# Kernel tuning notes

Measured on AMD Instinct MI355X. Metric: run time of the kernel, lower is better.

Reference implementation:

```python
import jax, jax.numpy as jnp
import numpy as np

O = 100000   # num objects
R = 1000000  # num triplets
D = 128      # per-slot feature dim (input_dim[0]=input_dim[1]=input_dim[2])
SUM_D = 3 * D  # MLP in/out width
H = 256      # hidden_dim


def setup_inputs() -> dict:
    key = jax.random.key(0)
    k1, k2, k3, k4, k5 = jax.random.split(key, 5)
    object_feats = jax.random.normal(k1, (O, D), dtype=jnp.float32)
    relation_feats = jax.random.normal(k2, (R, D), dtype=jnp.float32)
    triplet = jax.random.randint(k3, (R, 3), 0, O, dtype=jnp.int64)
    # MLP: Linear(SUM_D->H) + ReLU + Linear(H->SUM_D), kaiming-normal init
    W1 = jax.random.normal(k4, (SUM_D, H), dtype=jnp.float32) * np.sqrt(2.0 / SUM_D)
    b1 = jnp.zeros((H,), dtype=jnp.float32)
    W2 = jax.random.normal(k5, (H, SUM_D), dtype=jnp.float32) * np.sqrt(2.0 / H)
    b2 = jnp.zeros((SUM_D,), dtype=jnp.float32)
    return {
        "object_feats": object_feats,
        "relation_feats": relation_feats,
        "W1": W1, "b1": b1, "W2": W2, "b2": b2,
        "triplet": triplet,
        "triplet_len": R,
    }


def reference(object_feats, relation_feats, W1, b1, W2, b2, triplet, triplet_len):
    t = triplet[:triplet_len]                      # [R, 3]
    subs = t[:, 0]                                 # [R]
    objs = t[:, 1]                                 # [R]
    # gather subj/obj feats, concat with relation feats -> [R, 3D]
    gcn_feat = jnp.concatenate(
        [object_feats[subs], relation_feats, object_feats[objs]], axis=1)
    # 2-layer MLP
    h = jax.nn.relu(gcn_feat @ W1 + b1)            # [R, H]
    out = h @ W2 + b2                              # [R, 3D]
    sub_out = out[:, :D]
    rel_out = out[:, D:-D]
    obj_out = out[:, -D:]
    # scatter-add back to object nodes, then mean by degree, plus residual
    acc = jnp.zeros_like(object_feats)
    acc = acc.at[subs].add(sub_out).at[objs].add(obj_out)   # [O, D]
    one = jnp.ones((triplet_len,), dtype=object_feats.dtype)
    cnt = jnp.zeros((object_feats.shape[0],), dtype=object_feats.dtype)
    cnt = cnt.at[subs].add(one).at[objs].add(one)           # [O]
    output_feat = acc / jnp.clip(cnt, 1.0)[:, None] + object_feats
    return (output_feat, rel_out, triplet, triplet_len)
```

## Files before the change

### kernel.cpp

```cpp
#include <hip/hip_runtime.h>

#define O_N 100000
#define R_N 1000000
#define DIM 128
#define SD 384
#define HD 256
#define BR 64
#define NT (R_N / BR)
#define OBJ8 (O_N * DIM / 8)

typedef __attribute__((ext_vector_type(8))) short short8;
typedef __attribute__((ext_vector_type(4))) float f32x4;

static __device__ __forceinline__ unsigned short f2bf(float x) {
    union { float f; unsigned int u; } v; v.f = x;
    unsigned int r = v.u + 0x7FFFu + ((v.u >> 16) & 1u);
    return (unsigned short)(r >> 16);
}
static __device__ __forceinline__ unsigned long long pack4(f32x4 v) {
    return  (unsigned long long)f2bf(v.x)
         | ((unsigned long long)f2bf(v.y) << 16)
         | ((unsigned long long)f2bf(v.z) << 32)
         | ((unsigned long long)f2bf(v.w) << 48);
}

__global__ void prep_weights(const float* __restrict__ W1, const float* __restrict__ W2,
                             unsigned short* __restrict__ W1T, unsigned short* __restrict__ W2T) {
    int i = blockIdx.x * 256 + threadIdx.x;
    if (i < SD * HD) {
        int h = i / SD, k = i - h * SD;
        W1T[i] = f2bf(W1[k * HD + h]);
    } else {
        int j = i - SD * HD;
        int c = j / HD, k = j - c * HD;
        W2T[j] = f2bf(W2[k * SD + c]);
    }
}

__global__ void conv_obj(const float* __restrict__ objF, unsigned short* __restrict__ objBF) {
    int i = blockIdx.x * 256 + threadIdx.x;
    if (i < OBJ8) {
        f32x4 v0 = ((const f32x4*)(objF + (size_t)i * 8))[0];
        f32x4 v1 = ((const f32x4*)(objF + (size_t)i * 8))[1];
        unsigned long long* dd = (unsigned long long*)(objBF + (size_t)i * 8);
        dd[0] = pack4(v0);
        dd[1] = pack4(v1);
    }
}

__global__ void trip_cnt(const int* __restrict__ trip, float* __restrict__ tripOut,
                         float* __restrict__ lenOut, float* __restrict__ cnt,
                         const int* __restrict__ tlen) {
    int i = blockIdx.x * 256 + threadIdx.x;
    if (i < R_N) {
        int s = trip[3 * i], o = trip[3 * i + 1], t2 = trip[3 * i + 2];
        tripOut[3 * i]     = (float)s;
        tripOut[3 * i + 1] = (float)o;
        tripOut[3 * i + 2] = (float)t2;
        atomicAdd(&cnt[min(max(s, 0), O_N - 1)], 1.0f);
        atomicAdd(&cnt[min(max(o, 0), O_N - 1)], 1.0f);
        if (i == 0) lenOut[0] = (float)tlen[0];
    }
}

__global__ __launch_bounds__(256, 3)
void gemm1_kernel(const unsigned short* __restrict__ objBF, const float* __restrict__ relF,
                  const unsigned short* __restrict__ W1T, const float* __restrict__ b1,
                  const int* __restrict__ trip, unsigned char* __restrict__ hbfB) {
    __shared__ __align__(16) unsigned char Xso[32768];
    __shared__ __align__(16) unsigned char Xsr[16384];
    __shared__ int idxBuf[128];

    const int tid  = threadIdx.x;
    const int lane = tid & 63;
    const int w    = tid >> 6;
    const int r0   = blockIdx.x * BR;
    const int l15  = lane & 15;
    const int l4   = lane >> 4;
    const int hW   = w * 64;

    if (tid < 2 * BR) {
        int rr = r0 + (tid & (BR - 1));
        idxBuf[tid] = min(max(trip[3 * rr + (tid >> 6)], 0), O_N - 1);
    }
    __syncthreads();

    #pragma unroll
    for (int it = 0; it < 8; ++it) {
        int a   = it * 256 + tid;
        int row = a >> 5;
        int q   = a & 31;
        int u   = q ^ (row & 15);
        const unsigned short* src =
            objBF + (size_t)((q < 16) ? idxBuf[row] : idxBuf[BR + row]) * DIM + (u & 15) * 8;
        __builtin_amdgcn_global_load_lds(
            (const __attribute__((address_space(1))) void*)src,
            (__attribute__((address_space(3))) void*)(Xso + it * 4096 + w * 1024),
            16, 0, 0);
    }
    #pragma unroll
    for (int it = 0; it < 4; ++it) {
        int a2  = it * 256 + tid;
        int row = a2 >> 4;
        int j   = a2 & 15;
        const float* rp = relF + (size_t)(r0 + row) * DIM + j * 8;
        f32x4 v0 = ((const f32x4*)rp)[0];
        f32x4 v1 = ((const f32x4*)rp)[1];
        union { unsigned long long q[2]; short8 v; } u;
        u.q[0] = pack4(v0); u.q[1] = pack4(v1);
        *(short8*)(Xsr + row * 256 + ((j ^ (row & 15)) << 4)) = u.v;
    }
    __syncthreads();

    f32x4 acc1[4][4];
    #pragma unroll
    for (int a = 0; a < 4; ++a)
        #pragma unroll
        for (int b = 0; b < 4; ++b) acc1[a][b] = (f32x4)0.0f;

    #pragma unroll
    for (int ks = 0; ks < 12; ++ks) {
        int k0 = ks * 32;
        short8 af[4], bfr[4];
        #pragma unroll
        for (int mh = 0; mh < 4; ++mh)
            af[mh] = *(const short8*)(W1T + (hW + mh * 16 + l15) * SD + k0 + 8 * l4);
        #pragma unroll
        for (int nr = 0; nr < 4; ++nr) {
            int rel = nr * 16 + l15;
            int sw  = rel & 15;
            const unsigned char* p;
            if (ks < 4)       p = Xso + rel * 512 + (((ks * 4 + l4) ^ sw) << 4);
            else if (ks < 8)  p = Xsr + rel * 256 + ((((ks - 4) * 4 + l4) ^ sw) << 4);
            else              p = Xso + rel * 512 + 256 + ((((ks - 8) * 4 + l4) ^ sw) << 4);
            bfr[nr] = *(const short8*)p;
        }
        #pragma unroll
        for (int mh = 0; mh < 4; ++mh)
            #pragma unroll
            for (int nr = 0; nr < 4; ++nr)
                acc1[mh][nr] = __builtin_amdgcn_mfma_f32_16x16x32_bf16(
                    af[mh], bfr[nr], acc1[mh][nr], 0, 0, 0);
    }

    #pragma unroll
    for (int mh = 0; mh < 4; ++mh) {
        int hbase = hW + mh * 16 + 4 * l4;
        float bb0 = b1[hbase], bb1 = b1[hbase + 1], bb2 = b1[hbase + 2], bb3 = b1[hbase + 3];
        int hb   = hbase >> 3;
        int half = (hbase >> 2) & 1;
        #pragma unroll
        for (int nr = 0; nr < 4; ++nr) {
            int rel = nr * 16 + l15;
            unsigned long long pk =
                  (unsigned long long)f2bf(fmaxf(acc1[mh][nr][0] + bb0, 0.f))
                | ((unsigned long long)f2bf(fmaxf(acc1[mh][nr][1] + bb1, 0.f)) << 16)
                | ((unsigned long long)f2bf(fmaxf(acc1[mh][nr][2] + bb2, 0.f)) << 32)
                | ((unsigned long long)f2bf(fmaxf(acc1[mh][nr][3] + bb3, 0.f)) << 48);
            *(unsigned long long*)(hbfB + (size_t)(r0 + rel) * 512
                                   + ((hb ^ (rel & 15)) << 4) + half * 8) = pk;
        }
    }
}

__global__ __launch_bounds__(256, 3)
void gemm2_kernel(const unsigned char* __restrict__ hbfB,
                  const unsigned short* __restrict__ W2T, const float* __restrict__ b2,
                  const int* __restrict__ trip,
                  float* __restrict__ accB, float* __restrict__ relOut) {
    __shared__ __align__(16) unsigned char Hs[32768];
    __shared__ int idxBuf[128];

    const int tid  = threadIdx.x;
    const int lane = tid & 63;
    const int w    = tid >> 6;
    const int r0   = blockIdx.x * BR;
    const int l15  = lane & 15;
    const int l4   = lane >> 4;
    const int cW   = w * 96;

    if (tid < 2 * BR) {
        int rr = r0 + (tid & (BR - 1));
        idxBuf[tid] = min(max(trip[3 * rr + (tid >> 6)], 0), O_N - 1);
    }
    #pragma unroll
    for (int it = 0; it < 8; ++it) {
        const unsigned char* src = hbfB + (size_t)r0 * 512 + (size_t)(it * 256 + tid) * 16;
        __builtin_amdgcn_global_load_lds(
            (const __attribute__((address_space(1))) void*)src,
            (__attribute__((address_space(3))) void*)(Hs + it * 4096 + w * 1024),
            16, 0, 0);
    }
    __syncthreads();

    f32x4 acc2[4][6];
    #pragma unroll
    for (int a = 0; a < 4; ++a)
        #pragma unroll
        for (int b = 0; b < 6; ++b) acc2[a][b] = (f32x4)0.0f;

    #pragma unroll
    for (int ks = 0; ks < 8; ++ks) {
        int k0 = ks * 32;
        short8 ha[4], wb[6];
        #pragma unroll
        for (int ma = 0; ma < 4; ++ma) {
            int rel = ma * 16 + l15;
            int hb  = (k0 >> 3) + l4;
            ha[ma] = *(const short8*)(Hs + rel * 512 + ((hb ^ (rel & 15)) << 4));
        }
        #pragma unroll
        for (int nb = 0; nb < 6; ++nb) {
            int c = cW + nb * 16 + l15;
            wb[nb] = *(const short8*)(W2T + c * HD + k0 + 8 * l4);
        }
        #pragma unroll
        for (int ma = 0; ma < 4; ++ma)
            #pragma unroll
            for (int nb = 0; nb < 6; ++nb)
                acc2[ma][nb] = __builtin_amdgcn_mfma_f32_16x16x32_bf16(
                    ha[ma], wb[nb], acc2[ma][nb], 0, 0, 0);
    }

    #pragma unroll
    for (int ma = 0; ma < 4; ++ma) {
        int rloc = ma * 16 + 4 * l4;
        int rg   = r0 + rloc;
        int subs[4], objs[4];
        #pragma unroll
        for (int q = 0; q < 4; ++q) {
            subs[q] = idxBuf[rloc + q];
            objs[q] = idxBuf[BR + rloc + q];
        }
        #pragma unroll
        for (int nb = 0; nb < 6; ++nb) {
            int c = cW + nb * 16 + l15;
            float b2v = b2[c];
            #pragma unroll
            for (int q = 0; q < 4; ++q) {
                float v = acc2[ma][nb][q] + b2v;
                if (c < DIM) {
                    atomicAdd(accB + (size_t)subs[q] * DIM + c, v);
                } else if (c < 2 * DIM) {
                    relOut[(size_t)(rg + q) * DIM + (c - DIM)] = v;
                } else {
                    atomicAdd(accB + (size_t)objs[q] * DIM + (c - 2 * DIM), v);
                }
            }
        }
    }
}

__global__ void finalize(const float* __restrict__ accB, const float* __restrict__ cnt,
                         const float* __restrict__ objF, float* __restrict__ outF) {
    int i = blockIdx.x * 256 + threadIdx.x;
    if (i < O_N * DIM / 4) {
        int row = i >> 5;
        float c = fmaxf(cnt[row], 1.0f);
        f32x4 a = ((const f32x4*)accB)[i];
        f32x4 o = ((const f32x4*)objF)[i];
        f32x4 r;
        r.x = a.x / c + o.x;
        r.y = a.y / c + o.y;
        r.z = a.z / c + o.z;
        r.w = a.w / c + o.w;
        ((f32x4*)outF)[i] = r;
    }
}

extern "C" void kernel_launch(void* const* d_in, const int* in_sizes, int n_in,
                              void* d_out, int out_size, void* d_ws, size_t ws_size,
                              hipStream_t stream) {
    const float* objF = (const float*)d_in[0];
    const float* relF = (const float*)d_in[1];
    const float* W1   = (const float*)d_in[2];
    const float* b1   = (const float*)d_in[3];
    const float* W2   = (const float*)d_in[4];
    const float* b2   = (const float*)d_in[5];
    const int*   trip = (const int*)d_in[6];
    const int*   tlen = (const int*)d_in[7];

    float* outF    = (float*)d_out;
    float* relOut  = outF + (size_t)O_N * DIM;
    float* tripOut = relOut + (size_t)R_N * DIM;
    float* lenOut  = tripOut + (size_t)R_N * 3;

    unsigned short* W1T = (unsigned short*)d_ws;
    unsigned short* W2T = W1T + SD * HD;
    float* accB = (float*)(W2T + SD * HD);
    float* cnt  = accB + (size_t)O_N * DIM;
    unsigned short* objBF = (unsigned short*)(cnt + O_N);

    (void)hipMemsetAsync(accB, 0, ((size_t)O_N * DIM + O_N) * sizeof(float), stream);
    prep_weights<<<(2 * SD * HD) / 256, 256, 0, stream>>>(W1, W2, W1T, W2T);
    conv_obj<<<(OBJ8 + 255) / 256, 256, 0, stream>>>(objF, objBF);
    trip_cnt<<<(R_N + 255) / 256, 256, 0, stream>>>(trip, tripOut, lenOut, cnt, tlen);
    gemm1_kernel<<<NT, 256, 0, stream>>>(objBF, relF, W1T, b1, trip, (unsigned char*)relOut);
    gemm2_kernel<<<NT, 256, 0, stream>>>((const unsigned char*)relOut, W2T, b2, trip, accB, relOut);
    finalize<<<(O_N * DIM / 4 + 255) / 256, 256, 0, stream>>>(accB, cnt, objF, outF);
}
```

Baseline: 1.637 ms.

## Accumulate scatter-add in bf16 with packed atomics and transposed MFMA output

Changes the per-object accumulator from fp32 to bf16 and scatters sub/obj outputs with global_atomic_pk_add_bf16, so each atomic adds two values and the accumulator takes half the memory. The MFMA operands are swapped so each lane holds four consecutive columns of one row. This allows vectorized bias loads, float4 stores of the relation output, and packed atomics. The finalize kernel now reads bf16. The cost is lower accumulation precision: each object sums about 20 contributions in bf16, which may exceed the accuracy tolerance.

```diff
diff --git a/kernel.cpp b/kernel.cpp
--- a/kernel.cpp
+++ b/kernel.cpp
@@ -11,17 +11,26 @@
 
 typedef __attribute__((ext_vector_type(8))) short short8;
 typedef __attribute__((ext_vector_type(4))) float f32x4;
+typedef __attribute__((ext_vector_type(4))) unsigned short bfu16x4;
 
 static __device__ __forceinline__ unsigned short f2bf(float x) {
     union { float f; unsigned int u; } v; v.f = x;
     unsigned int r = v.u + 0x7FFFu + ((v.u >> 16) & 1u);
     return (unsigned short)(r >> 16);
+}
+static __device__ __forceinline__ float bf2f(unsigned short b) {
+    union { unsigned int u; float f; } v; v.u = ((unsigned int)b) << 16;
+    return v.f;
 }
 static __device__ __forceinline__ unsigned long long pack4(f32x4 v) {
     return  (unsigned long long)f2bf(v.x)
          | ((unsigned long long)f2bf(v.y) << 16)
          | ((unsigned long long)f2bf(v.z) << 32)
          | ((unsigned long long)f2bf(v.w) << 48);
+}
+static __device__ __forceinline__ void atomic_pk_bf16(unsigned short* p, unsigned int pk) {
+    unsigned long long addr = (unsigned long long)p;
+    asm volatile("global_atomic_pk_add_bf16 %0, %1, off" : : "v"(addr), "v"(pk) : "memory");
 }
 
 __global__ void prep_weights(const float* __restrict__ W1, const float* __restrict__ W2,
@@ -167,7 +176,7 @@
 void gemm2_kernel(const unsigned char* __restrict__ hbfB,
                   const unsigned short* __restrict__ W2T, const float* __restrict__ b2,
                   const int* __restrict__ trip,
-                  float* __restrict__ accB, float* __restrict__ relOut) {
+                  unsigned short* __restrict__ accB, float* __restrict__ relOut) {
     __shared__ __align__(16) unsigned char Hs[32768];
     __shared__ int idxBuf[128];
 
@@ -193,11 +202,11 @@
     }
     __syncthreads();
 
-    f32x4 acc2[4][6];
-    #pragma unroll
-    for (int a = 0; a < 4; ++a)
-        #pragma unroll
-        for (int b = 0; b < 6; ++b) acc2[a][b] = (f32x4)0.0f;
+    f32x4 acc2[6][4];
+    #pragma unroll
+    for (int a = 0; a < 6; ++a)
+        #pragma unroll
+        for (int b = 0; b < 4; ++b) acc2[a][b] = (f32x4)0.0f;
 
     #pragma unroll
     for (int ks = 0; ks < 8; ++ks) {
@@ -215,55 +224,54 @@
             wb[nb] = *(const short8*)(W2T + c * HD + k0 + 8 * l4);
         }
         #pragma unroll
-        for (int ma = 0; ma < 4; ++ma)
+        for (int nb = 0; nb < 6; ++nb)
             #pragma unroll
-            for (int nb = 0; nb < 6; ++nb)
-                acc2[ma][nb] = __builtin_amdgcn_mfma_f32_16x16x32_bf16(
-                    ha[ma], wb[nb], acc2[ma][nb], 0, 0, 0);
-    }
-
-    #pragma unroll
-    for (int ma = 0; ma < 4; ++ma) {
-        int rloc = ma * 16 + 4 * l4;
-        int rg   = r0 + rloc;
-        int subs[4], objs[4];
-        #pragma unroll
-        for (int q = 0; q < 4; ++q) {
-            subs[q] = idxBuf[rloc + q];
-            objs[q] = idxBuf[BR + rloc + q];
-        }
-        #pragma unroll
-        for (int nb = 0; nb < 6; ++nb) {
-            int c = cW + nb * 16 + l15;
-            float b2v = b2[c];
-            #pragma unroll
-            for (int q = 0; q < 4; ++q) {
-                float v = acc2[ma][nb][q] + b2v;
-                if (c < DIM) {
-                    atomicAdd(accB + (size_t)subs[q] * DIM + c, v);
-                } else if (c < 2 * DIM) {
-                    relOut[(size_t)(rg + q) * DIM + (c - DIM)] = v;
-                } else {
-                    atomicAdd(accB + (size_t)objs[q] * DIM + (c - 2 * DIM), v);
-                }
+            for (int ma = 0; ma < 4; ++ma)
+                acc2[nb][ma] = __builtin_amdgcn_mfma_f32_16x16x32_bf16(
+                    wb[nb], ha[ma], acc2[nb][ma], 0, 0, 0);
+    }
+
+    #pragma unroll
+    for (int nb = 0; nb < 6; ++nb) {
+        int cb = cW + nb * 16 + 4 * l4;
+        f32x4 b2v = *(const f32x4*)(b2 + cb);
+        #pragma unroll
+        for (int ma = 0; ma < 4; ++ma) {
+            int rel = ma * 16 + l15;
+            int rg  = r0 + rel;
+            f32x4 v;
+            v.x = acc2[nb][ma][0] + b2v.x;
+            v.y = acc2[nb][ma][1] + b2v.y;
+            v.z = acc2[nb][ma][2] + b2v.z;
+            v.w = acc2[nb][ma][3] + b2v.w;
+            if (cb < DIM) {
+                unsigned short* p = accB + (size_t)idxBuf[rel] * DIM + cb;
+                atomic_pk_bf16(p,     (unsigned int)f2bf(v.x) | ((unsigned int)f2bf(v.y) << 16));
+                atomic_pk_bf16(p + 2, (unsigned int)f2bf(v.z) | ((unsigned int)f2bf(v.w) << 16));
+            } else if (cb < 2 * DIM) {
+                *(f32x4*)(relOut + (size_t)rg * DIM + (cb - DIM)) = v;
+            } else {
+                unsigned short* p = accB + (size_t)idxBuf[BR + rel] * DIM + (cb - 2 * DIM);
+                atomic_pk_bf16(p,     (unsigned int)f2bf(v.x) | ((unsigned int)f2bf(v.y) << 16));
+                atomic_pk_bf16(p + 2, (unsigned int)f2bf(v.z) | ((unsigned int)f2bf(v.w) << 16));
             }
         }
     }
 }
 
-__global__ void finalize(const float* __restrict__ accB, const float* __restrict__ cnt,
+__global__ void finalize(const unsigned short* __restrict__ accB, const float* __restrict__ cnt,
                          const float* __restrict__ objF, float* __restrict__ outF) {
     int i = blockIdx.x * 256 + threadIdx.x;
     if (i < O_N * DIM / 4) {
         int row = i >> 5;
         float c = fmaxf(cnt[row], 1.0f);
-        f32x4 a = ((const f32x4*)accB)[i];
+        bfu16x4 a = *(const bfu16x4*)(accB + (size_t)i * 4);
         f32x4 o = ((const f32x4*)objF)[i];
         f32x4 r;
-        r.x = a.x / c + o.x;
-        r.y = a.y / c + o.y;
-        r.z = a.z / c + o.z;
-        r.w = a.w / c + o.w;
+        r.x = bf2f(a.x) / c + o.x;
+        r.y = bf2f(a.y) / c + o.y;
+        r.z = bf2f(a.z) / c + o.z;
+        r.w = bf2f(a.w) / c + o.w;
         ((f32x4*)outF)[i] = r;
     }
 }
@@ -287,11 +295,11 @@
 
     unsigned short* W1T = (unsigned short*)d_ws;
     unsigned short* W2T = W1T + SD * HD;
-    float* accB = (float*)(W2T + SD * HD);
-    float* cnt  = accB + (size_t)O_N * DIM;
+    unsigned short* accB = W2T + SD * HD;
+    float* cnt = (float*)(accB + (size_t)O_N * DIM);
     unsigned short* objBF = (unsigned short*)(cnt + O_N);
 
-    (void)hipMemsetAsync(accB, 0, ((size_t)O_N * DIM + O_N) * sizeof(float), stream);
+    (void)hipMemsetAsync(accB, 0, (size_t)O_N * DIM * 2 + (size_t)O_N * 4, stream);
     prep_weights<<<(2 * SD * HD) / 256, 256, 0, stream>>>(W1, W2, W1T, W2T);
     conv_obj<<<(OBJ8 + 255) / 256, 256, 0, stream>>>(objF, objBF);
     trip_cnt<<<(R_N + 255) / 256, 256, 0, stream>>>(trip, tripOut, lenOut, cnt, tlen);
```

Result: slower. 2.406 ms (+46.9%).
